# Performance work log

Hardware: AMD Instinct MI355X
Metric: run time of the kernel (lower is better)

The kernel has to match this reference:

```python
import jax, jax.numpy as jnp
import numpy as np

# config (matches init_kwargs)
NA, NEN = 8, 8            # n_agents, n_enemies
NENT = NA + NEN           # n_entities
NFA, NFE = 64, 64         # state_nf_al, state_nf_en
E, A, M, HE = 64, 64, 32, 64  # entity_embed, attn_embed, mixing_embed, hypernet_embed
TD, TE = 64, 64           # task_repre_dim, task_repre_embed_dim
BS, SL = 64, 512


def setup_inputs() -> dict:
    key = jax.random.key(0)
    ks = iter(jax.random.split(key, 32))
    def rn(shape, scale=0.05):
        return jax.random.normal(next(ks), shape, dtype=jnp.float32) * scale
    return {
        "agent_qs": rn((BS, SL, NA), 1.0),
        "states": rn((BS, SL, NA * NFA + NEN * NFE), 1.0),
        "task_repre_mu": rn((BS, SL, NA, TD), 1.0),
        "ally_w": rn((NFA, E)), "ally_b": rn((E,)),
        "enemy_w": rn((NFE, E)), "enemy_b": rn((E,)),
        "q_w": rn((E, A)), "q_b": rn((A,)),
        "k_w": rn((E, A)), "k_b": rn((A,)),
        "hw1_w1": rn((E + NFA + TE, HE)), "hw1_b1": rn((HE,)),
        "hw1_w2": rn((HE, M)), "hw1_b2": rn((M,)),
        "hwf_w1": rn((E + TE, HE)), "hwf_b1": rn((HE,)),
        "hwf_w2": rn((HE, M)), "hwf_b2": rn((M,)),
        "hb1_w": rn((E + TE, M)), "hb1_b": rn((M,)),
        "v_w1": rn((E + TE, M)), "v_b1": rn((M,)),
        "v_w2": rn((M, 1)), "v_b2": rn((1,)),
        "tre_w": rn((TD, TE)), "tre_b": rn((TE,)),
    }


def reference(agent_qs, states, task_repre_mu,
              ally_w, ally_b, enemy_w, enemy_b,
              q_w, q_b, k_w, k_b,
              hw1_w1, hw1_b1, hw1_w2, hw1_b2,
              hwf_w1, hwf_b1, hwf_w2, hwf_b2,
              hb1_w, hb1_b, v_w1, v_b1, v_w2, v_b2,
              tre_w, tre_b):
    bs, sl = agent_qs.shape[:2]
    # decompose_state (state_last_action=False, state_timestep_number=False)
    ally = states[..., : NA * NFA].reshape(bs, sl, NA, NFA)      # [bs,sl,NA,NFA]
    enemy = states[..., NA * NFA:].reshape(bs, sl, NEN, NFE)     # [bs,sl,NEN,NFE]
    ally_e = ally @ ally_w + ally_b                              # [bs,sl,NA,E]
    enemy_e = enemy @ enemy_w + enemy_b                          # [bs,sl,NEN,E]
    ent = jnp.concatenate([ally_e, enemy_e], axis=2)             # [bs,sl,NENT,E]
    q = ent @ q_w + q_b                                          # [bs,sl,NENT,A]
    k = ent @ k_w + k_b
    energy = jnp.einsum('bsqa,bska->bsqk', q, k)                 # [bs,sl,NENT,NENT]
    # torch: F.softmax(energy, dim=1) on [B,n_ent,n_ent] -> softmax over query axis
    attn = jax.nn.softmax(energy, axis=2)
    # attn_out = bmm(value[B,E,n], attn[B,n,n]).mean(-1)
    attn_out = jnp.einsum('bsne,bsnk->bse', ent, attn) / NENT    # [bs,sl,E]

    mean_mu = task_repre_mu.mean(axis=-2)                        # [bs,sl,TD]
    tre = task_repre_mu @ tre_w + tre_b                          # [bs,sl,NA,TE]
    mean_tre = mean_mu @ tre_w + tre_b                           # [bs,sl,TE]

    ent_mix = jnp.concatenate([
        jnp.broadcast_to(attn_out[:, :, None, :], (bs, sl, NA, E)),
        ally, tre], axis=-1)                                     # [bs,sl,NA,E+NFA+TE]
    mix = jnp.concatenate([attn_out, mean_tre], axis=-1)         # [bs,sl,E+TE]

    w1 = jnp.abs(jax.nn.relu(ent_mix @ hw1_w1 + hw1_b1) @ hw1_w2 + hw1_b2)  # [bs,sl,NA,M]
    b1 = mix @ hb1_w + hb1_b                                     # [bs,sl,M]
    hidden = jax.nn.elu(jnp.einsum('bsn,bsnm->bsm', agent_qs, w1) + b1)     # [bs,sl,M]
    wf = jnp.abs(jax.nn.relu(mix @ hwf_w1 + hwf_b1) @ hwf_w2 + hwf_b2)      # [bs,sl,M]
    v = jax.nn.relu(mix @ v_w1 + v_b1) @ v_w2 + v_b2             # [bs,sl,1]
    q_tot = jnp.einsum('bsm,bsm->bs', hidden, wf)[..., None] + v # [bs,sl,1]
    return q_tot
```

## Files before the change

### kernel.cpp

```cpp
#include <hip/hip_runtime.h>
#include <math.h>


#define TOKS 32768

typedef __attribute__((ext_vector_type(8))) short short8;
typedef __attribute__((ext_vector_type(4))) float f32x4;

#define MFMA(a, b, c) __builtin_amdgcn_mfma_f32_16x16x32_bf16((a), (b), (c), 0, 0, 0)

#define E_CAT   0
#define E_WQKT  8192
#define E_ZBRT  13312
#define E_H1T   29696
#define E_W2T   41984
#define E_WFT   44032
#define E_BF16_TOTAL 46080
#define E_AO_US 46464

__device__ __forceinline__ unsigned short bfr(float x) {
    unsigned u = __builtin_bit_cast(unsigned, x);
    u += 0x7fffu + ((u >> 16) & 1u);
    return (unsigned short)(u >> 16);
}
__device__ __forceinline__ float bf2f(unsigned short h) {
    unsigned u = ((unsigned)h) << 16;
    return __builtin_bit_cast(float, u);
}
__device__ __forceinline__ short8 cvt8v(float4 a, float4 b) {
    short8 r;
    r[0] = (short)bfr(a.x); r[1] = (short)bfr(a.y);
    r[2] = (short)bfr(a.z); r[3] = (short)bfr(a.w);
    r[4] = (short)bfr(b.x); r[5] = (short)bfr(b.y);
    r[6] = (short)bfr(b.z); r[7] = (short)bfr(b.w);
    return r;
}
#define SWZ64(r, c)  ((((r) * 64)  + (c)) ^ (((r) & 7) << 3))
#define SWZ128(r, c) ((((r) * 128) + (c)) ^ (((r) & 7) << 3))
#define SWZ192(r, c) ((((r) * 192) + (c)) ^ (((r) & 7) << 3))

__global__ __launch_bounds__(256) void qmix_setup(
    const float* __restrict__ ally_w, const float* __restrict__ enemy_w,
    const float* __restrict__ q_w, const float* __restrict__ k_w,
    const float* __restrict__ k_b,
    const float* __restrict__ hw1_w1, const float* __restrict__ hw1_b1,
    const float* __restrict__ hw1_w2,
    const float* __restrict__ hwf_w1, const float* __restrict__ hwf_b1,
    const float* __restrict__ hwf_w2,
    const float* __restrict__ hb1_w, const float* __restrict__ hb1_b,
    const float* __restrict__ v_w1, const float* __restrict__ v_b1,
    const float* __restrict__ tre_w, const float* __restrict__ tre_b,
    unsigned short* __restrict__ wsb, float* __restrict__ wsf)
{
    int gid = blockIdx.x * 256 + threadIdx.x;
    if (gid < E_BF16_TOTAL) {
        float v = 0.f;
        int base, r, c, K;
        if (gid < E_WQKT) {
            base = E_CAT; K = 128;
            int i = gid - base; r = i >> 7; c = i & 127;
            v = (c < 64) ? ally_w[c * 64 + r] : enemy_w[(c - 64) * 64 + r];
        } else if (gid < E_ZBRT) {
            base = E_WQKT; K = 64;
            int i = gid - base; r = i >> 6; c = i & 63;
            if (r < 64) {
                for (int g = 0; g < 64; ++g) v += q_w[c * 64 + g] * k_w[r * 64 + g];
            } else if (r == 64) {
                for (int g = 0; g < 64; ++g) v += q_w[c * 64 + g] * k_b[g];
            }
        } else if (gid < E_H1T) {
            base = E_ZBRT; K = 128;
            int i = gid - base; r = i >> 7; c = i & 127;
            if (r < 64) {
                if (c < 64) v = hwf_w1[c * 64 + r];
                else for (int g = 0; g < 64; ++g) v += tre_w[(c - 64) * 64 + g] * hwf_w1[(64 + g) * 64 + r];
            } else if (r < 96) {
                int m = r - 64;
                if (c < 64) v = hb1_w[c * 32 + m];
                else for (int g = 0; g < 64; ++g) v += tre_w[(c - 64) * 64 + g] * hb1_w[(64 + g) * 32 + m];
            } else {
                int m = r - 96;
                if (c < 64) v = v_w1[c * 32 + m];
                else for (int g = 0; g < 64; ++g) v += tre_w[(c - 64) * 64 + g] * v_w1[(64 + g) * 32 + m];
            }
        } else if (gid < E_W2T) {
            base = E_H1T; K = 192;
            int i = gid - base; r = i / 192; c = i % 192;
            if (c < 64) v = hw1_w1[(64 + c) * 64 + r];
            else if (c < 128) {
                for (int g = 0; g < 64; ++g) v += tre_w[(c - 64) * 64 + g] * hw1_w1[(128 + g) * 64 + r];
            } else v = hw1_w1[(c - 128) * 64 + r];
        } else if (gid < E_WFT) {
            base = E_W2T; K = 64;
            int i = gid - base; r = i >> 6; c = i & 63;
            v = hw1_w2[c * 32 + r];
        } else {
            base = E_WFT; K = 64;
            int i = gid - base; r = i >> 6; c = i & 63;
            v = hwf_w2[c * 32 + r];
        }
        wsb[base + ((r * K + c) ^ ((r & 7) << 3))] = bfr(v);
    } else if (gid < E_BF16_TOTAL + 192) {
        int j = gid - E_BF16_TOTAL; float v;
        if (j < 64) {
            v = hw1_b1[j];
            for (int g = 0; g < 64; ++g) v += tre_b[g] * hw1_w1[(128 + g) * 64 + j];
        } else if (j < 128) {
            int e = j - 64; v = hwf_b1[e];
            for (int g = 0; g < 64; ++g) v += tre_b[g] * hwf_w1[(64 + g) * 64 + e];
        } else if (j < 160) {
            int m = j - 128; v = hb1_b[m];
            for (int g = 0; g < 64; ++g) v += tre_b[g] * hb1_w[(64 + g) * 32 + m];
        } else {
            int m = j - 160; v = v_b1[m];
            for (int g = 0; g < 64; ++g) v += tre_b[g] * v_w1[(64 + g) * 32 + m];
        }
        wsf[j] = v;
    }
}

__global__ __launch_bounds__(512) void qmix_attn(
    const float* __restrict__ states,
    const float* __restrict__ ally_b, const float* __restrict__ enemy_b,
    const unsigned short* __restrict__ wsb,
    unsigned short* __restrict__ aoG)
{
    __shared__ unsigned short sWa[13312];
    __shared__ unsigned short sE[8][1024];
    __shared__ unsigned short sT[8][1024];

    const int lane = threadIdx.x & 63;
    const int wv   = threadIdx.x >> 6;
    const int l15  = lane & 15;
    const int lg   = lane >> 4;
    const int kb   = lg * 8;
    const size_t t = (size_t)blockIdx.x * 8 + wv;

    const short8 zero8 = {0, 0, 0, 0, 0, 0, 0, 0};
    const f32x4  zero4 = {0.f, 0.f, 0.f, 0.f};

    for (int i = threadIdx.x * 8; i < 13312; i += 512 * 8)
        *(short8*)(sWa + i) = *(const short8*)(wsb + E_CAT + i);

    const int roff = (l15 < 8) ? (l15 * 64 + kb) : (512 + (l15 - 8) * 64 + kb);
    const float* p = states + t * 1024 + roff;
    float4 cur0 = *(const float4*)(p);
    float4 cur1 = *(const float4*)(p + 4);
    float4 cur2 = *(const float4*)(p + 32);
    float4 cur3 = *(const float4*)(p + 36);

    float biasEnt[4];
    #pragma unroll
    for (int nt = 0; nt < 4; ++nt) {
        int col = nt * 16 + l15;
        biasEnt[nt] = (lg < 2) ? ally_b[col] : enemy_b[col];
    }
    __syncthreads();
    const unsigned short* lCAT  = sWa;
    const unsigned short* lWQKT = sWa + 8192;

    unsigned short* E = sE[wv];
    unsigned short* T = sT[wv];

    short8 a01 = cvt8v(cur0, cur1);
    short8 a23 = cvt8v(cur2, cur3);
    const bool isally = (l15 < 8);

    f32x4 accB[4] = {zero4, zero4, zero4, zero4};
    #pragma unroll
    for (int ks = 0; ks < 4; ++ks) {
        short8 af;
        if (ks == 0)      af = isally ? a01 : zero8;
        else if (ks == 1) af = isally ? a23 : zero8;
        else if (ks == 2) af = isally ? zero8 : a01;
        else              af = isally ? zero8 : a23;
        #pragma unroll
        for (int nt = 0; nt < 4; ++nt) {
            short8 w = *(const short8*)&lCAT[SWZ128(nt * 16 + l15, ks * 32 + kb)];
            accB[nt] = MFMA(af, w, accB[nt]);
        }
    }
    float entv[4][4];
    #pragma unroll
    for (int nt = 0; nt < 4; ++nt) {
        #pragma unroll
        for (int reg = 0; reg < 4; ++reg) {
            entv[nt][reg] = accB[nt][reg] + biasEnt[nt];
            E[SWZ64(lg * 4 + reg, nt * 16 + l15)] = bfr(entv[nt][reg]);
        }
    }

    f32x4 accC[5] = {zero4, zero4, zero4, zero4, zero4};
    short8 ef0 = *(const short8*)&E[SWZ64(l15, 0 * 32 + kb)];
    short8 ef1 = *(const short8*)&E[SWZ64(l15, 1 * 32 + kb)];
    #pragma unroll
    for (int nt = 0; nt < 5; ++nt) {
        short8 w0 = *(const short8*)&lWQKT[SWZ64(nt * 16 + l15, 0 * 32 + kb)];
        short8 w1 = *(const short8*)&lWQKT[SWZ64(nt * 16 + l15, 1 * 32 + kb)];
        accC[nt] = MFMA(ef0, w0, accC[nt]);
        accC[nt] = MFMA(ef1, w1, accC[nt]);
    }
    const int src = lane & 48;
    float si[4];
    #pragma unroll
    for (int reg = 0; reg < 4; ++reg) si[reg] = __shfl(accC[4][reg], src);
    #pragma unroll
    for (int nt = 0; nt < 4; ++nt)
        #pragma unroll
        for (int reg = 0; reg < 4; ++reg)
            T[SWZ64(lg * 4 + reg, nt * 16 + l15)] = bfr(accC[nt][reg]);

    f32x4 en = zero4;
    {
        short8 ta0 = *(const short8*)&T[SWZ64(l15, 0 * 32 + kb)];
        short8 ta1 = *(const short8*)&T[SWZ64(l15, 1 * 32 + kb)];
        en = MFMA(ta0, ef0, en);
        en = MFMA(ta1, ef1, en);
    }
    #pragma unroll
    for (int reg = 0; reg < 4; ++reg) en[reg] += si[reg];

    float mx = fmaxf(fmaxf(en[0], en[1]), fmaxf(en[2], en[3]));
    mx = fmaxf(mx, __shfl_xor(mx, 16));
    mx = fmaxf(mx, __shfl_xor(mx, 32));
    float p0 = __expf(en[0] - mx), p1 = __expf(en[1] - mx);
    float p2 = __expf(en[2] - mx), p3 = __expf(en[3] - mx);
    float s = p0 + p1 + p2 + p3;
    s += __shfl_xor(s, 16);
    s += __shfl_xor(s, 32);
    float inv = 1.f / s;
    float r0 = p0 * inv, r1 = p1 * inv, r2 = p2 * inv, r3 = p3 * inv;
    r0 += __shfl_xor(r0, 1); r0 += __shfl_xor(r0, 2); r0 += __shfl_xor(r0, 4); r0 += __shfl_xor(r0, 8);
    r1 += __shfl_xor(r1, 1); r1 += __shfl_xor(r1, 2); r1 += __shfl_xor(r1, 4); r1 += __shfl_xor(r1, 8);
    r2 += __shfl_xor(r2, 1); r2 += __shfl_xor(r2, 2); r2 += __shfl_xor(r2, 4); r2 += __shfl_xor(r2, 8);
    r3 += __shfl_xor(r3, 1); r3 += __shfl_xor(r3, 2); r3 += __shfl_xor(r3, 4); r3 += __shfl_xor(r3, 8);

    float part[4];
    #pragma unroll
    for (int nt = 0; nt < 4; ++nt) {
        float pp = r0 * entv[nt][0] + r1 * entv[nt][1]
                 + r2 * entv[nt][2] + r3 * entv[nt][3];
        pp += __shfl_xor(pp, 16);
        pp += __shfl_xor(pp, 32);
        part[nt] = pp;
    }
    float ao = (lg == 0) ? part[0] : (lg == 1) ? part[1]
             : (lg == 2) ? part[2] : part[3];
    aoG[t * 64 + lane] = bfr(ao * 0.0625f);
}

__global__ __launch_bounds__(256) void qmix_hyper(
    const float* __restrict__ agent_qs, const float* __restrict__ states,
    const float* __restrict__ mu,
    const float* __restrict__ v_w2, const float* __restrict__ v_b2,
    const float* __restrict__ hw1_b2, const float* __restrict__ hwf_b2,
    const unsigned short* __restrict__ wsb, const float* __restrict__ wsf,
    const unsigned short* __restrict__ aoG,
    float* __restrict__ out)
{
    __shared__ unsigned short sWb[16384];
    __shared__ unsigned short sZ[4][1024];
    __shared__ unsigned short sH1all[8192];
    __shared__ float sB1[4][512];
    __shared__ float sWF[4][512];
    __shared__ float sV[4][16];

    const int tid  = threadIdx.x;
    const int lane = tid & 63;
    const int wv   = tid >> 6;
    const int l15  = lane & 15;
    const int lg   = lane >> 4;
    const int kb   = lg * 8;
    const int T0   = blockIdx.x * 64 + wv * 16;
    const int tokB = blockIdx.x * 64;

    const float* BH1 = wsf + 0;
    const float* BHF = wsf + 64;
    const float* BB1 = wsf + 128;
    const float* BV  = wsf + 160;

    const f32x4 zero4 = {0.f, 0.f, 0.f, 0.f};

    for (int i = tid * 8; i < 16384; i += 256 * 8)
        *(short8*)(sWb + i) = *(const short8*)(wsb + E_ZBRT + i);

    short8 zA0 = *(const short8*)&aoG[(size_t)(T0 + l15) * 64 + kb];
    short8 zA1 = *(const short8*)&aoG[(size_t)(T0 + l15) * 64 + 32 + kb];

    #pragma unroll
    for (int tg = 0; tg < 64; tg += 32) {
        int tok = tg + (tid >> 3);
        int e8  = (tid & 7) * 8;
        const float* mp = mu + (size_t)(tokB + tok) * 512 + e8;
        float s0 = 0.f, s1 = 0.f, s2 = 0.f, s3 = 0.f,
              s4 = 0.f, s5 = 0.f, s6 = 0.f, s7 = 0.f;
        #pragma unroll
        for (int a = 0; a < 8; ++a) {
            float4 u = *(const float4*)(mp + a * 64);
            float4 v = *(const float4*)(mp + a * 64 + 4);
            s0 += u.x; s1 += u.y; s2 += u.z; s3 += u.w;
            s4 += v.x; s5 += v.y; s6 += v.z; s7 += v.w;
        }
        short8 r;
        r[0] = (short)bfr(s0 * 0.125f); r[1] = (short)bfr(s1 * 0.125f);
        r[2] = (short)bfr(s2 * 0.125f); r[3] = (short)bfr(s3 * 0.125f);
        r[4] = (short)bfr(s4 * 0.125f); r[5] = (short)bfr(s5 * 0.125f);
        r[6] = (short)bfr(s6 * 0.125f); r[7] = (short)bfr(s7 * 0.125f);
        *(short8*)&sH1all[SWZ64(tok, e8)] = r;
    }
    __syncthreads();

    f32x4 zb[8] = {zero4, zero4, zero4, zero4, zero4, zero4, zero4, zero4};
    #pragma unroll
    for (int ks = 0; ks < 4; ++ks) {
        short8 af;
        if (ks == 0)      af = zA0;
        else if (ks == 1) af = zA1;
        else af = *(const short8*)&sH1all[SWZ64(wv * 16 + l15, (ks - 2) * 32 + kb)];
        #pragma unroll
        for (int nt = 0; nt < 8; ++nt) {
            short8 w = *(const short8*)&sWb[SWZ128(nt * 16 + l15, ks * 32 + kb)];
            zb[nt] = MFMA(af, w, zb[nt]);
        }
    }
    __syncthreads();

    for (int i = tid * 8; i < 16384; i += 256 * 8)
        *(short8*)(sWb + i) = *(const short8*)(wsb + E_H1T + i);

    #pragma unroll
    for (int nt = 0; nt < 4; ++nt) {
        int col = nt * 16 + l15;
        float bz = BHF[col];
        #pragma unroll
        for (int reg = 0; reg < 4; ++reg)
            sZ[wv][SWZ64(lg * 4 + reg, col)] = bfr(fmaxf(zb[nt][reg] + bz, 0.f));
    }
    #pragma unroll
    for (int nt = 4; nt < 6; ++nt) {
        int m = (nt - 4) * 16 + l15;
        float bb = BB1[m];
        #pragma unroll
        for (int reg = 0; reg < 4; ++reg)
            sB1[wv][(lg * 4 + reg) * 32 + m] = zb[nt][reg] + bb;
    }
    {
        float bv0 = BV[l15], bv1 = BV[16 + l15];
        float vw0 = v_w2[l15], vw1 = v_w2[16 + l15];
        #pragma unroll
        for (int reg = 0; reg < 4; ++reg) {
            float vp = fmaxf(zb[6][reg] + bv0, 0.f) * vw0
                     + fmaxf(zb[7][reg] + bv1, 0.f) * vw1;
            vp += __shfl_xor(vp, 1); vp += __shfl_xor(vp, 2);
            vp += __shfl_xor(vp, 4); vp += __shfl_xor(vp, 8);
            if (l15 == 0) sV[wv][lg * 4 + reg] = vp;
        }
    }
    __syncthreads();
    const unsigned short* lH1T = sWb;
    const unsigned short* lW2T = sWb + 12288;
    const unsigned short* lWFT = sWb + 14336;
    unsigned short* tile = sH1all + wv * 2048;

    {
        f32x4 wfa = zero4, wfb = zero4;
        #pragma unroll
        for (int ks = 0; ks < 2; ++ks) {
            short8 af = *(const short8*)&sZ[wv][SWZ64(l15, ks * 32 + kb)];
            short8 b0 = *(const short8*)&lWFT[SWZ64(l15, ks * 32 + kb)];
            short8 b1 = *(const short8*)&lWFT[SWZ64(16 + l15, ks * 32 + kb)];
            wfa = MFMA(af, b0, wfa);
            wfb = MFMA(af, b1, wfb);
        }
        float hb0 = hwf_b2[l15], hb1 = hwf_b2[16 + l15];
        #pragma unroll
        for (int reg = 0; reg < 4; ++reg) {
            int tok = lg * 4 + reg;
            sWF[wv][tok * 32 + l15]      = fabsf(wfa[reg] + hb0);
            sWF[wv][tok * 32 + 16 + l15] = fabsf(wfb[reg] + hb1);
        }
    }

    const float vb2 = v_b2[0];
    const float b20 = hw1_b2[l15], b21 = hw1_b2[16 + l15];
    const int agent = l15 & 7;
    const int toff  = l15 >> 3;

    float4 cs0, cs1, cs2, cs3, cm0, cm1, cm2, cm3;
    short8 ca0, ca1;
    {
        const size_t tokA = (size_t)(T0 + toff);
        const float* sp = states + tokA * 1024 + agent * 64 + kb;
        const float* mp = mu + tokA * 512 + agent * 64 + kb;
        cs0 = *(const float4*)sp;        cs1 = *(const float4*)(sp + 4);
        cs2 = *(const float4*)(sp + 32); cs3 = *(const float4*)(sp + 36);
        cm0 = *(const float4*)mp;        cm1 = *(const float4*)(mp + 4);
        cm2 = *(const float4*)(mp + 32); cm3 = *(const float4*)(mp + 36);
        ca0 = *(const short8*)&aoG[tokA * 64 + kb];
        ca1 = *(const short8*)&aoG[tokA * 64 + 32 + kb];
    }

    for (int mc = 0; mc < 8; ++mc) {
        float4 us0 = cs0, us1 = cs1, us2 = cs2, us3 = cs3;
        float4 um0 = cm0, um1 = cm1, um2 = cm2, um3 = cm3;
        short8 ua0 = ca0, ua1 = ca1;
        if (mc < 7) {
            const size_t tokA = (size_t)(T0 + (mc + 1) * 2 + toff);
            const float* sp = states + tokA * 1024 + agent * 64 + kb;
            const float* mp = mu + tokA * 512 + agent * 64 + kb;
            cs0 = *(const float4*)sp;        cs1 = *(const float4*)(sp + 4);
            cs2 = *(const float4*)(sp + 32); cs3 = *(const float4*)(sp + 36);
            cm0 = *(const float4*)mp;        cm1 = *(const float4*)(mp + 4);
            cm2 = *(const float4*)(mp + 32); cm3 = *(const float4*)(mp + 36);
            ca0 = *(const short8*)&aoG[tokA * 64 + kb];
            ca1 = *(const short8*)&aoG[tokA * 64 + 32 + kb];
        }
        short8 f0 = cvt8v(us0, us1), f1 = cvt8v(us2, us3);
        short8 f2 = cvt8v(um0, um1), f3 = cvt8v(um2, um3);

        f32x4 h[4] = {zero4, zero4, zero4, zero4};
        #pragma unroll
        for (int ks = 0; ks < 6; ++ks) {
            short8 af = (ks == 0) ? f0 : (ks == 1) ? f1 : (ks == 2) ? f2
                      : (ks == 3) ? f3 : (ks == 4) ? ua0 : ua1;
            #pragma unroll
            for (int nt = 0; nt < 4; ++nt) {
                short8 w = *(const short8*)&lH1T[SWZ192(nt * 16 + l15, ks * 32 + kb)];
                h[nt] = MFMA(af, w, h[nt]);
            }
        }
        #pragma unroll
        for (int nt = 0; nt < 4; ++nt) {
            int col = nt * 16 + l15;
            float bh = BH1[col];
            #pragma unroll
            for (int reg = 0; reg < 4; ++reg)
                tile[SWZ64(lg * 4 + reg, col)] = bfr(fmaxf(h[nt][reg] + bh, 0.f));
        }

        f32x4 wa = zero4, wb = zero4;
        #pragma unroll
        for (int ks = 0; ks < 2; ++ks) {
            short8 af = *(const short8*)&tile[SWZ64(l15, ks * 32 + kb)];
            short8 b0 = *(const short8*)&lW2T[SWZ64(l15, ks * 32 + kb)];
            short8 b1 = *(const short8*)&lW2T[SWZ64(16 + l15, ks * 32 + kb)];
            wa = MFMA(af, b0, wa);
            wb = MFMA(af, b1, wb);
        }

        float hp0 = 0.f, hp1 = 0.f;
        #pragma unroll
        for (int reg = 0; reg < 4; ++reg) {
            int row = lg * 4 + reg;
            float qsv = agent_qs[(size_t)(T0 + mc * 2 + (row >> 3)) * 8 + (row & 7)];
            hp0 += qsv * fabsf(wa[reg] + b20);
            hp1 += qsv * fabsf(wb[reg] + b21);
        }
        hp0 += __shfl_xor(hp0, 16);
        hp1 += __shfl_xor(hp1, 16);
        int tokL = mc * 2 + (lg >> 1);
        float e0 = hp0 + sB1[wv][tokL * 32 + l15];
        float e1 = hp1 + sB1[wv][tokL * 32 + 16 + l15];
        float hid0 = e0 > 0.f ? e0 : (__expf(e0) - 1.f);
        float hid1 = e1 > 0.f ? e1 : (__expf(e1) - 1.f);
        float q = hid0 * sWF[wv][tokL * 32 + l15]
                + hid1 * sWF[wv][tokL * 32 + 16 + l15];
        q += __shfl_xor(q, 1); q += __shfl_xor(q, 2);
        q += __shfl_xor(q, 4); q += __shfl_xor(q, 8);
        if (l15 == 0 && (lg & 1) == 0)
            out[T0 + tokL] = q + sV[wv][tokL] + vb2;
    }
}

extern "C" void kernel_launch(void* const* d_in, const int* in_sizes, int n_in,
                              void* d_out, int out_size, void* d_ws, size_t ws_size,
                              hipStream_t stream)
{
    const float* agent_qs = (const float*)d_in[0];
    const float* states   = (const float*)d_in[1];
    const float* mu       = (const float*)d_in[2];
    const float* ally_w   = (const float*)d_in[3];
    const float* ally_b   = (const float*)d_in[4];
    const float* enemy_w  = (const float*)d_in[5];
    const float* enemy_b  = (const float*)d_in[6];
    const float* q_w      = (const float*)d_in[7];
    const float* k_w      = (const float*)d_in[9];
    const float* k_b      = (const float*)d_in[10];
    const float* hw1_w1   = (const float*)d_in[11];
    const float* hw1_b1   = (const float*)d_in[12];
    const float* hw1_w2   = (const float*)d_in[13];
    const float* hw1_b2   = (const float*)d_in[14];
    const float* hwf_w1   = (const float*)d_in[15];
    const float* hwf_b1   = (const float*)d_in[16];
    const float* hwf_w2   = (const float*)d_in[17];
    const float* hwf_b2   = (const float*)d_in[18];
    const float* hb1_w    = (const float*)d_in[19];
    const float* hb1_b    = (const float*)d_in[20];
    const float* v_w1     = (const float*)d_in[21];
    const float* v_b1     = (const float*)d_in[22];
    const float* v_w2     = (const float*)d_in[23];
    const float* v_b2     = (const float*)d_in[24];
    const float* tre_w    = (const float*)d_in[25];
    const float* tre_b    = (const float*)d_in[26];

    unsigned short* wsb = (unsigned short*)d_ws;
    float* wsf = (float*)((char*)d_ws + (size_t)E_BF16_TOTAL * 2);
    unsigned short* aoG = wsb + E_AO_US;
    float* out = (float*)d_out;

    hipLaunchKernelGGL(qmix_setup, dim3(181), dim3(256), 0, stream,
                       ally_w, enemy_w, q_w, k_w, k_b,
                       hw1_w1, hw1_b1, hw1_w2,
                       hwf_w1, hwf_b1, hwf_w2,
                       hb1_w, hb1_b, v_w1, v_b1, tre_w, tre_b,
                       wsb, wsf);

    hipLaunchKernelGGL(qmix_attn, dim3(TOKS / 8), dim3(512), 0, stream,
                       states, ally_b, enemy_b, wsb, aoG);

    hipLaunchKernelGGL(qmix_hyper, dim3(TOKS / 64), dim3(256), 0, stream,
                       agent_qs, states, mu, v_w2, v_b2, hw1_b2, hwf_b2,
                       wsb, wsf, aoG, out);
}
```

Measured before the change: 94.23 us.

## Split hyper kernel work across eight waves of eight tokens each

Doubles the hyper kernel block to 512 threads so each wavefront handles 8 tokens instead of 16, halving the per-wave main loop and raising parallelism. The first-stage MFMAs now run with half the A rows zeroed, and shared buffers are reorganised to fit eight per-wave tiles. This wastes half of the small-stage MFMA throughput and raises register and LDS pressure per block, in exchange for more waves to hide memory latency. The diff also leaves an unused scoped variable.

```diff
diff --git a/kernel.cpp b/kernel.cpp
--- a/kernel.cpp
+++ b/kernel.cpp
@@ -249,7 +249,7 @@
     aoG[t * 64 + lane] = bfr(ao * 0.0625f);
 }
 
-__global__ __launch_bounds__(256) void qmix_hyper(
+__global__ __launch_bounds__(512) void qmix_hyper(
     const float* __restrict__ agent_qs, const float* __restrict__ states,
     const float* __restrict__ mu,
     const float* __restrict__ v_w2, const float* __restrict__ v_b2,
@@ -259,11 +259,11 @@
     float* __restrict__ out)
 {
     __shared__ unsigned short sWb[16384];
-    __shared__ unsigned short sZ[4][1024];
-    __shared__ unsigned short sH1all[8192];
-    __shared__ float sB1[4][512];
-    __shared__ float sWF[4][512];
-    __shared__ float sV[4][16];
+    __shared__ unsigned short sMM[8192];
+    __shared__ unsigned short sZT[8][1024];
+    __shared__ float sB1[8][256];
+    __shared__ float sWF[8][256];
+    __shared__ float sV[8][8];
 
     const int tid  = threadIdx.x;
     const int lane = tid & 63;
@@ -271,7 +271,7 @@
     const int l15  = lane & 15;
     const int lg   = lane >> 4;
     const int kb   = lg * 8;
-    const int T0   = blockIdx.x * 64 + wv * 16;
+    const int T0   = blockIdx.x * 64 + wv * 8;
     const int tokB = blockIdx.x * 64;
 
     const float* BH1 = wsf + 0;
@@ -279,17 +279,20 @@
     const float* BB1 = wsf + 128;
     const float* BV  = wsf + 160;
 
-    const f32x4 zero4 = {0.f, 0.f, 0.f, 0.f};
-
-    for (int i = tid * 8; i < 16384; i += 256 * 8)
+    const short8 zero8 = {0, 0, 0, 0, 0, 0, 0, 0};
+    const f32x4  zero4 = {0.f, 0.f, 0.f, 0.f};
+
+    for (int i = tid * 8; i < 16384; i += 512 * 8)
         *(short8*)(sWb + i) = *(const short8*)(wsb + E_ZBRT + i);
 
-    short8 zA0 = *(const short8*)&aoG[(size_t)(T0 + l15) * 64 + kb];
-    short8 zA1 = *(const short8*)&aoG[(size_t)(T0 + l15) * 64 + 32 + kb];
-
-    #pragma unroll
-    for (int tg = 0; tg < 64; tg += 32) {
-        int tok = tg + (tid >> 3);
+    {
+        const size_t row = (size_t)(T0 + (l15 & 7));
+    }
+    short8 zA0 = *(const short8*)&aoG[(size_t)(T0 + (l15 & 7)) * 64 + kb];
+    short8 zA1 = *(const short8*)&aoG[(size_t)(T0 + (l15 & 7)) * 64 + 32 + kb];
+
+    {
+        int tok = tid >> 3;
         int e8  = (tid & 7) * 8;
         const float* mp = mu + (size_t)(tokB + tok) * 512 + e8;
         float s0 = 0.f, s1 = 0.f, s2 = 0.f, s3 = 0.f,
@@ -306,17 +309,22 @@
         r[2] = (short)bfr(s2 * 0.125f); r[3] = (short)bfr(s3 * 0.125f);
         r[4] = (short)bfr(s4 * 0.125f); r[5] = (short)bfr(s5 * 0.125f);
         r[6] = (short)bfr(s6 * 0.125f); r[7] = (short)bfr(s7 * 0.125f);
-        *(short8*)&sH1all[SWZ64(tok, e8)] = r;
-    }
+        *(short8*)&sMM[SWZ64(tok, e8)] = r;
+    }
+    for (int i = lane; i < 512; i += 64) sZT[wv][512 + i] = 0;
     __syncthreads();
 
     f32x4 zb[8] = {zero4, zero4, zero4, zero4, zero4, zero4, zero4, zero4};
+    const bool arow = (l15 < 8);
     #pragma unroll
     for (int ks = 0; ks < 4; ++ks) {
         short8 af;
-        if (ks == 0)      af = zA0;
-        else if (ks == 1) af = zA1;
-        else af = *(const short8*)&sH1all[SWZ64(wv * 16 + l15, (ks - 2) * 32 + kb)];
+        if (ks == 0)      af = arow ? zA0 : zero8;
+        else if (ks == 1) af = arow ? zA1 : zero8;
+        else {
+            short8 m = *(const short8*)&sMM[SWZ64(wv * 8 + (l15 & 7), (ks - 2) * 32 + kb)];
+            af = arow ? m : zero8;
+        }
         #pragma unroll
         for (int nt = 0; nt < 8; ++nt) {
             short8 w = *(const short8*)&sWb[SWZ128(nt * 16 + l15, ks * 32 + kb)];
@@ -325,24 +333,26 @@
     }
     __syncthreads();
 
-    for (int i = tid * 8; i < 16384; i += 256 * 8)
+    for (int i = tid * 8; i < 16384; i += 512 * 8)
         *(short8*)(sWb + i) = *(const short8*)(wsb + E_H1T + i);
 
-    #pragma unroll
-    for (int nt = 0; nt < 4; ++nt) {
-        int col = nt * 16 + l15;
-        float bz = BHF[col];
-        #pragma unroll
-        for (int reg = 0; reg < 4; ++reg)
-            sZ[wv][SWZ64(lg * 4 + reg, col)] = bfr(fmaxf(zb[nt][reg] + bz, 0.f));
-    }
-    #pragma unroll
-    for (int nt = 4; nt < 6; ++nt) {
-        int m = (nt - 4) * 16 + l15;
-        float bb = BB1[m];
-        #pragma unroll
-        for (int reg = 0; reg < 4; ++reg)
-            sB1[wv][(lg * 4 + reg) * 32 + m] = zb[nt][reg] + bb;
+    if (lg < 2) {
+        #pragma unroll
+        for (int nt = 0; nt < 4; ++nt) {
+            int col = nt * 16 + l15;
+            float bz = BHF[col];
+            #pragma unroll
+            for (int reg = 0; reg < 4; ++reg)
+                sZT[wv][SWZ64(lg * 4 + reg, col)] = bfr(fmaxf(zb[nt][reg] + bz, 0.f));
+        }
+        #pragma unroll
+        for (int nt = 4; nt < 6; ++nt) {
+            int m = (nt - 4) * 16 + l15;
+            float bb = BB1[m];
+            #pragma unroll
+            for (int reg = 0; reg < 4; ++reg)
+                sB1[wv][(lg * 4 + reg) * 32 + m] = zb[nt][reg] + bb;
+        }
     }
     {
         float bv0 = BV[l15], bv1 = BV[16 + l15];
@@ -353,31 +363,32 @@
                      + fmaxf(zb[7][reg] + bv1, 0.f) * vw1;
             vp += __shfl_xor(vp, 1); vp += __shfl_xor(vp, 2);
             vp += __shfl_xor(vp, 4); vp += __shfl_xor(vp, 8);
-            if (l15 == 0) sV[wv][lg * 4 + reg] = vp;
+            if (l15 == 0 && lg < 2) sV[wv][lg * 4 + reg] = vp;
         }
     }
     __syncthreads();
     const unsigned short* lH1T = sWb;
     const unsigned short* lW2T = sWb + 12288;
     const unsigned short* lWFT = sWb + 14336;
-    unsigned short* tile = sH1all + wv * 2048;
 
     {
         f32x4 wfa = zero4, wfb = zero4;
         #pragma unroll
         for (int ks = 0; ks < 2; ++ks) {
-            short8 af = *(const short8*)&sZ[wv][SWZ64(l15, ks * 32 + kb)];
+            short8 af = *(const short8*)&sZT[wv][SWZ64(l15, ks * 32 + kb)];
             short8 b0 = *(const short8*)&lWFT[SWZ64(l15, ks * 32 + kb)];
             short8 b1 = *(const short8*)&lWFT[SWZ64(16 + l15, ks * 32 + kb)];
             wfa = MFMA(af, b0, wfa);
             wfb = MFMA(af, b1, wfb);
         }
-        float hb0 = hwf_b2[l15], hb1 = hwf_b2[16 + l15];
-        #pragma unroll
-        for (int reg = 0; reg < 4; ++reg) {
-            int tok = lg * 4 + reg;
-            sWF[wv][tok * 32 + l15]      = fabsf(wfa[reg] + hb0);
-            sWF[wv][tok * 32 + 16 + l15] = fabsf(wfb[reg] + hb1);
+        if (lg < 2) {
+            float hb0 = hwf_b2[l15], hb1 = hwf_b2[16 + l15];
+            #pragma unroll
+            for (int reg = 0; reg < 4; ++reg) {
+                int tok = lg * 4 + reg;
+                sWF[wv][tok * 32 + l15]      = fabsf(wfa[reg] + hb0);
+                sWF[wv][tok * 32 + 16 + l15] = fabsf(wfb[reg] + hb1);
+            }
         }
     }
 
@@ -385,6 +396,7 @@
     const float b20 = hw1_b2[l15], b21 = hw1_b2[16 + l15];
     const int agent = l15 & 7;
     const int toff  = l15 >> 3;
+    unsigned short* tile = sZT[wv];
 
     float4 cs0, cs1, cs2, cs3, cm0, cm1, cm2, cm3;
     short8 ca0, ca1;
@@ -400,11 +412,11 @@
         ca1 = *(const short8*)&aoG[tokA * 64 + 32 + kb];
     }
 
-    for (int mc = 0; mc < 8; ++mc) {
+    for (int mc = 0; mc < 4; ++mc) {
         float4 us0 = cs0, us1 = cs1, us2 = cs2, us3 = cs3;
         float4 um0 = cm0, um1 = cm1, um2 = cm2, um3 = cm3;
         short8 ua0 = ca0, ua1 = ca1;
-        if (mc < 7) {
+        if (mc < 3) {
             const size_t tokA = (size_t)(T0 + (mc + 1) * 2 + toff);
             const float* sp = states + tokA * 1024 + agent * 64 + kb;
             const float* mp = mu + tokA * 512 + agent * 64 + kb;
@@ -518,7 +530,7 @@
     hipLaunchKernelGGL(qmix_attn, dim3(TOKS / 8), dim3(512), 0, stream,
                        states, ally_b, enemy_b, wsb, aoG);
 
-    hipLaunchKernelGGL(qmix_hyper, dim3(TOKS / 64), dim3(256), 0, stream,
+    hipLaunchKernelGGL(qmix_hyper, dim3(TOKS / 64), dim3(512), 0, stream,
                        agent_qs, states, mu, v_w2, v_b2, hw1_b2, hwf_b2,
                        wsb, wsf, aoG, out);
 }
```

Result: faster. 88.72 us (-5.9%).
